# Performance work log

Hardware: AMD Instinct MI355X
Metric: run time of the kernel (lower is better)

Reference implementation:

```python
import jax, jax.numpy as jnp
import numpy as np

PATCH = 14
DIM = 512
LEVELS = 6
ITERS = LEVELS * 2  # default iters
TOKEN_ATTEND_SELF_VALUE = -0.0005


def setup_inputs() -> dict:
    key = jax.random.key(0)
    ks = jax.random.split(key, 9)
    b = 8
    # weights scaled down (~1/sqrt(dim)) so 12 iterations stay finite in fp32
    s = 0.02
    return {
        "img": jax.random.normal(ks[0], (b, 3, 224, 224), jnp.float32),
        "W_patch": jax.random.normal(ks[1], (PATCH * PATCH * 3, DIM), jnp.float32) * s,
        "b_patch": jax.random.normal(ks[2], (DIM,), jnp.float32) * s,
        "pos_emb": jax.random.normal(ks[3], (256, DIM), jnp.float32) * s,
        "init_levels": jax.random.normal(ks[4], (LEVELS, DIM), jnp.float32),
        "bu_in": jax.random.normal(ks[5], (LEVELS - 1, DIM, 4 * DIM), jnp.float32) * s,
        "bu_out": jax.random.normal(ks[6], (LEVELS - 1, 4 * DIM, DIM), jnp.float32) * s,
        "td_in": jax.random.normal(ks[7], (LEVELS - 1, DIM, 4 * DIM), jnp.float32) * s,
        "td_out": jax.random.normal(ks[8], (LEVELS - 1, 4 * DIM, DIM), jnp.float32) * s,
    }


def _grouped_ff(x, w_in, w_out):
    # x: [b, n, groups, d]; per-group two-layer FF with exact GELU
    h = jnp.einsum('bnld,lde->bnle', x, w_in)
    h = jax.nn.gelu(h, approximate=False)
    return jnp.einsum('bnld,lde->bnle', h, w_out)


def _consensus(levels):
    # levels: [b, n, l, d]; attend_self=False, no local radius
    n, d = levels.shape[1], levels.shape[-1]
    norm = jnp.maximum(jnp.linalg.norm(levels, axis=-1, keepdims=True), 1e-12)
    k = levels / norm
    sim = jnp.einsum('bild,bjld->blij', levels, k) * (d ** -0.5)
    eye = jnp.eye(n, dtype=bool)[None, None]
    sim = jnp.where(eye, jnp.asarray(TOKEN_ATTEND_SELF_VALUE, sim.dtype), sim)
    attn = jax.nn.softmax(sim, axis=-1)
    return jnp.einsum('blij,bjld->bild', attn, levels)


def reference(img, W_patch, b_patch, pos_emb, init_levels, bu_in, bu_out, td_in, td_out):
    b, c, H, W = img.shape
    p = PATCH
    h, w = H // p, W // p
    # 'b c (h p1) (w p2) -> b (h w) (p1 p2 c)'
    x = img.reshape(b, c, h, p, w, p).transpose(0, 2, 4, 3, 5, 1).reshape(b, h * w, p * p * c)
    tokens = x @ W_patch + b_patch  # [b, n, d]
    n = tokens.shape[1]
    pos = pos_emb[:n][None, :, None, :]       # [1, n, 1, d]
    bottom = tokens[:, :, None, :]            # [b, n, 1, d]
    levels = jnp.broadcast_to(init_levels[None, None], (b, n, LEVELS, DIM))

    for _ in range(ITERS):
        lwi = jnp.concatenate([bottom, levels], axis=2)            # [b, n, L+1, d]
        bu = _grouped_ff(lwi[:, :, 1:-1], bu_in, bu_out)           # [b, n, L-1, d]
        td = _grouped_ff(lwi[:, :, 2:] + pos, td_in, td_out)       # [b, n, L-1, d]
        bu = jnp.concatenate([bottom, bu], axis=2)                 # [b, n, L, d]
        td = jnp.pad(td, ((0, 0), (0, 0), (0, 1), (0, 0)))         # [b, n, L, d]
        cons = _consensus(levels)
        levels = (levels + bu + td + cons) * 0.25
    return levels
```

## Files before the change

### kernel.cpp

```cpp
#include <hip/hip_runtime.h>
#include <hip/hip_bf16.h>
#include <math.h>

#define B_   8
#define N_   256
#define L_   6
#define D_   512
#define NT_  2048
#define HID_ 2048

typedef __attribute__((ext_vector_type(4))) float f32x4;
typedef __attribute__((ext_vector_type(8))) short bf16x8;

struct bf16x4s { __hip_bfloat16 x, y, z, w; };

__device__ __forceinline__ bf16x4s to_bf4(float a, float b, float c, float d) {
    bf16x4s r;
    r.x = __float2bfloat16(a); r.y = __float2bfloat16(b);
    r.z = __float2bfloat16(c); r.w = __float2bfloat16(d);
    return r;
}

__device__ __forceinline__ float bf_to_f(unsigned short u) {
    union { unsigned int i; float f; } c;
    c.i = ((unsigned int)u) << 16;
    return c.f;
}

__device__ __forceinline__ void gload16(const void* g, void* l) {
    __builtin_amdgcn_global_load_lds(
        (const __attribute__((address_space(1))) int*)g,
        (__attribute__((address_space(3))) int*)l, 16, 0, 0);
}

__device__ __forceinline__ float gelu_exact(float v) {
    return 0.5f * v * (1.0f + erff(v * 0.70710678118654752f));
}

template<int BM, int BN, int WM, int WN, typename CT, bool GELU>
__global__ __launch_bounds__(512, 4) void gemm_ff(
    const __hip_bfloat16* __restrict__ A1, int lda1, long az1,
    const __hip_bfloat16* __restrict__ A2, int lda2, long az2, int zsplit,
    const __hip_bfloat16* __restrict__ B, int ldb, long bz,
    CT* __restrict__ C, int ldc, long cz, int K)
{
    constexpr int WVM = BM / WM, WVN = BN / WN;
    constexpr int MR = WVM / 16, NR = WVN / 16;
    constexpr int ALOADS = (BM * 64) / (512 * 8);
    constexpr int BLOADS = (BN * 64) / (512 * 8);
    constexpr int LOADS  = ALOADS + BLOADS;

    __shared__ short As[2][BM * 64];
    __shared__ short Bs[2][BN * 64];

    const int tid = threadIdx.x;
    const int wv = tid >> 6, lane = tid & 63;
    const int wr = wv / WN, wc = wv % WN;

    const int gx = gridDim.x, gy = gridDim.y;
    const int nwg = gx * gy * gridDim.z;
    int lid = (blockIdx.z * gy + blockIdx.y) * gx + blockIdx.x;
    lid = (lid & 7) * (nwg >> 3) + (lid >> 3);
    const int bx = lid % gx, by = (lid / gx) % gy, bzz = lid / (gx * gy);

    const __hip_bfloat16* A;
    int lda;
    if (bzz < zsplit) { A = A1 + (long)bzz * az1;            lda = lda1; }
    else              { A = A2 + (long)(bzz - zsplit) * az2; lda = lda2; }
    B += (long)bzz * bz;  C += (long)bzz * cz;
    const int m0 = by * BM, n0 = bx * BN;

    f32x4 acc[MR][NR] = {};

    const int srow_a = tid >> 3, sslot = tid & 7;

#define STAGE(BUF, K0)                                                        \
    {                                                                         \
        _Pragma("unroll")                                                     \
        for (int i = 0; i < ALOADS; ++i) {                                    \
            const int row = srow_a + i * 64;                                  \
            const int gs  = sslot ^ (row & 7);                                \
            gload16(A + (long)(m0 + row) * lda + (K0) + gs * 8,               \
                    &As[BUF][(wv * 64 + i * 512) * 8]);                       \
        }                                                                     \
        _Pragma("unroll")                                                     \
        for (int i = 0; i < BLOADS; ++i) {                                    \
            const int row = srow_a + i * 64;                                  \
            const int gs  = sslot ^ (row & 7);                                \
            gload16(B + (long)(n0 + row) * ldb + (K0) + gs * 8,               \
                    &Bs[BUF][(wv * 64 + i * 512) * 8]);                       \
        }                                                                     \
    }

    const int fr = lane & 15, k4 = lane >> 4;
    const int nt = K / 64;
    int cur = 0;

    STAGE(0, 0);

    for (int t = 0; t < nt; ++t) {
        if (t + 1 < nt) {
            STAGE(cur ^ 1, (t + 1) * 64);
            asm volatile("s_waitcnt vmcnt(%0)\n\ts_barrier"
                         :: "n"(LOADS) : "memory");
        } else {
            asm volatile("s_waitcnt vmcnt(0)\n\ts_barrier" ::: "memory");
        }

#pragma unroll
        for (int ks = 0; ks < 2; ++ks) {
            bf16x8 af[MR], bf[NR];
#pragma unroll
            for (int i = 0; i < MR; ++i) {
                const int r = wr * WVM + i * 16 + fr;
                af[i] = *(const bf16x8*)&As[cur][r * 64 + ((ks * 4 + k4) ^ (r & 7)) * 8];
            }
#pragma unroll
            for (int j = 0; j < NR; ++j) {
                const int r = wc * WVN + j * 16 + fr;
                bf[j] = *(const bf16x8*)&Bs[cur][r * 64 + ((ks * 4 + k4) ^ (r & 7)) * 8];
            }
            __builtin_amdgcn_s_setprio(1);
#pragma unroll
            for (int i = 0; i < MR; ++i)
#pragma unroll
                for (int j = 0; j < NR; ++j)
                    acc[i][j] = __builtin_amdgcn_mfma_f32_16x16x32_bf16(
                        af[i], bf[j], acc[i][j], 0, 0, 0);
            __builtin_amdgcn_s_setprio(0);
        }
        asm volatile("s_waitcnt lgkmcnt(0)\n\ts_barrier" ::: "memory");
        cur ^= 1;
    }
#undef STAGE

    const int cr4 = (lane >> 4) * 4, cc = lane & 15;
#pragma unroll
    for (int i = 0; i < MR; ++i)
#pragma unroll
        for (int j = 0; j < NR; ++j) {
            const int col = n0 + wc * WVN + j * 16 + cc;
#pragma unroll
            for (int r = 0; r < 4; ++r) {
                const int row = m0 + wr * WVM + i * 16 + cr4 + r;
                float v = acc[i][j][r];
                if (GELU) v = gelu_exact(v);
                CT* p = &C[(long)row * ldc + col];
                if constexpr (sizeof(CT) == 2) *p = __float2bfloat16(v);
                else *p = (CT)v;
            }
        }
}

__global__ __launch_bounds__(256) void simsm_kernel(
    const __hip_bfloat16* __restrict__ lev_bf, const float* __restrict__ invn,
    __hip_bfloat16* __restrict__ attn)
{
    __shared__ short As[64 * 32];
    __shared__ short Bs[256 * 32];
    __shared__ float redm[64][4];
    __shared__ float reds[64][4];

    const int tid = threadIdx.x;
    const int wv = tid >> 6, lane = tid & 63;
    const int z = blockIdx.y;
    const int b = z / 6, l = z - 6 * b;
    const __hip_bfloat16* base = lev_bf + (long)b * (N_ * L_ * D_) + (long)l * D_;
    const int m0 = blockIdx.x * 64;

    const int srow = tid >> 2, sslot = tid & 3;

    f32x4 acc[4][4] = {};
    const int fr = lane & 15, ksub = lane >> 4;

    for (int k0 = 0; k0 < 512; k0 += 32) {
        __syncthreads();
        {
            const int gs = sslot ^ ((srow >> 1) & 3);
            gload16(base + (long)(m0 + srow) * (L_ * D_) + k0 + gs * 8,
                    As + wv * 512);
        }
#pragma unroll
        for (int i = 0; i < 4; ++i) {
            const int row = srow + i * 64;
            const int gs  = sslot ^ ((row >> 1) & 3);
            gload16(base + (long)row * (L_ * D_) + k0 + gs * 8,
                    Bs + i * 2048 + wv * 512);
        }
        __syncthreads();

        bf16x8 af[4], bfr[4];
#pragma unroll
        for (int i = 0; i < 4; ++i) {
            const int ra = i * 16 + fr;
            af[i] = *(const bf16x8*)(As + ra * 32 + (ksub ^ ((ra >> 1) & 3)) * 8);
            const int rb = wv * 64 + i * 16 + fr;
            bfr[i] = *(const bf16x8*)(Bs + rb * 32 + (ksub ^ ((rb >> 1) & 3)) * 8);
        }
#pragma unroll
        for (int i = 0; i < 4; ++i)
#pragma unroll
            for (int j = 0; j < 4; ++j)
                acc[i][j] = __builtin_amdgcn_mfma_f32_16x16x32_bf16(
                    af[i], bfr[j], acc[i][j], 0, 0, 0);
    }

    const int cr4 = (lane >> 4) * 4, cc = lane & 15;
    const float sc = 0.044194173824159216f;

    float iv[4];
#pragma unroll
    for (int j = 0; j < 4; ++j)
        iv[j] = invn[((long)b * N_ + wv * 64 + j * 16 + cc) * L_ + l] * sc;
#pragma unroll
    for (int i = 0; i < 4; ++i)
#pragma unroll
        for (int j = 0; j < 4; ++j) {
            const int jg = wv * 64 + j * 16 + cc;
#pragma unroll
            for (int r = 0; r < 4; ++r) {
                const int ig = m0 + i * 16 + cr4 + r;
                float v = acc[i][j][r] * iv[j];
                if (ig == jg) v = -0.0005f;
                acc[i][j][r] = v;
            }
        }

    __syncthreads();

#pragma unroll
    for (int i = 0; i < 4; ++i)
#pragma unroll
        for (int r = 0; r < 4; ++r) {
            float m = fmaxf(fmaxf(acc[i][0][r], acc[i][1][r]),
                            fmaxf(acc[i][2][r], acc[i][3][r]));
#pragma unroll
            for (int o = 1; o < 16; o <<= 1) m = fmaxf(m, __shfl_xor(m, o));
            if (cc == 0) redm[i * 16 + cr4 + r][wv] = m;
        }
    __syncthreads();

#pragma unroll
    for (int i = 0; i < 4; ++i)
#pragma unroll
        for (int r = 0; r < 4; ++r) {
            const int rl = i * 16 + cr4 + r;
            const float m = fmaxf(fmaxf(redm[rl][0], redm[rl][1]),
                                  fmaxf(redm[rl][2], redm[rl][3]));
            float s = 0.f;
#pragma unroll
            for (int j = 0; j < 4; ++j) {
                const float e = expf(acc[i][j][r] - m);
                acc[i][j][r] = e;
                s += e;
            }
#pragma unroll
            for (int o = 1; o < 16; o <<= 1) s += __shfl_xor(s, o);
            if (cc == 0) reds[rl][wv] = s;
        }
    __syncthreads();

#pragma unroll
    for (int i = 0; i < 4; ++i)
#pragma unroll
        for (int r = 0; r < 4; ++r) {
            const int rl = i * 16 + cr4 + r;
            const float inv = 1.0f / (reds[rl][0] + reds[rl][1] +
                                      reds[rl][2] + reds[rl][3]);
            const long rowoff = ((long)z * N_ + m0 + rl) * N_;
#pragma unroll
            for (int j = 0; j < 4; ++j)
                attn[rowoff + wv * 64 + j * 16 + cc] =
                    __float2bfloat16(acc[i][j][r] * inv);
        }
}

__device__ __forceinline__ void mfma_kloop(
    const __hip_bfloat16* __restrict__ A, int lda,
    const __hip_bfloat16* __restrict__ B, int ldb,
    int m0, int n0, int K, short* As, short* Bs,
    f32x4 acc[4][4], int wave, int lane)
{
    const int srow_in = lane >> 2;
    const int sslot   = lane & 3;
    const int wm = (wave >> 1) * 64, wn = (wave & 1) * 64;

    for (int k0 = 0; k0 < K; k0 += 32) {
        __syncthreads();
#pragma unroll
        for (int c = 0; c < 2; ++c) {
            const int rbase = c * 64 + wave * 16;
            const int row   = rbase + srow_in;
            const int gk    = sslot ^ ((row >> 1) & 3);
            gload16(A + (long)(m0 + row) * lda + k0 + gk * 8, As + rbase * 32);
            gload16(B + (long)(n0 + row) * ldb + k0 + gk * 8, Bs + rbase * 32);
        }
        __syncthreads();

        const int fr = lane & 15, ksub = lane >> 4;
        bf16x8 af[4], bfr[4];
#pragma unroll
        for (int i = 0; i < 4; ++i) {
            const int ra = wm + i * 16 + fr;
            af[i]  = *(const bf16x8*)(As + ra * 32 + (ksub ^ ((ra >> 1) & 3)) * 8);
            const int rb = wn + i * 16 + fr;
            bfr[i] = *(const bf16x8*)(Bs + rb * 32 + (ksub ^ ((rb >> 1) & 3)) * 8);
        }
#pragma unroll
        for (int i = 0; i < 4; ++i)
#pragma unroll
            for (int j = 0; j < 4; ++j)
                acc[i][j] = __builtin_amdgcn_mfma_f32_16x16x32_bf16(
                    af[i], bfr[j], acc[i][j], 0, 0, 0);
    }
}

template<typename CT, bool GELU>
__global__ __launch_bounds__(256) void gemm_mfma(
    const __hip_bfloat16* __restrict__ A, int lda, long az,
    const __hip_bfloat16* __restrict__ B, int ldb, long bz,
    CT* __restrict__ C, int ldc, long cz, int K,
    const float* __restrict__ bias)
{
    __shared__ short As[128 * 32];
    __shared__ short Bs[128 * 32];
    const int tid = threadIdx.x;
    const int wave = tid >> 6, lane = tid & 63;
    const int z = blockIdx.z;
    A += (long)z * az;  B += (long)z * bz;  C += (long)z * cz;
    const int m0 = blockIdx.y * 128, n0 = blockIdx.x * 128;
    const int wm = (wave >> 1) * 64, wn = (wave & 1) * 64;

    f32x4 acc[4][4] = {};
    mfma_kloop(A, lda, B, ldb, m0, n0, K, As, Bs, acc, wave, lane);

    const int cr = lane >> 4, cc = lane & 15;
#pragma unroll
    for (int j = 0; j < 4; ++j) {
        const int col = n0 + wn + j * 16 + cc;
        const float bv = bias ? bias[col] : 0.f;
#pragma unroll
        for (int i = 0; i < 4; ++i)
#pragma unroll
            for (int r = 0; r < 4; ++r) {
                const int row = m0 + wm + i * 16 + cr * 4 + r;
                float v = acc[i][j][r] + bv;
                if (GELU) v = gelu_exact(v);
                CT* p = &C[(long)row * ldc + col];
                if constexpr (sizeof(CT) == 2) *p = __float2bfloat16(v);
                else *p = (CT)v;
            }
    }
}

__global__ __launch_bounds__(256) void cons_mfma(
    const __hip_bfloat16* __restrict__ attn, const __hip_bfloat16* __restrict__ levT,
    __hip_bfloat16* __restrict__ cons)
{
    __shared__ short As[128 * 32];
    __shared__ short Bs[128 * 32];
    const int tid = threadIdx.x;
    const int wave = tid >> 6, lane = tid & 63;
    const int z = blockIdx.z;
    const int b = z / 6, l = z - 6 * b;
    const __hip_bfloat16* A = attn + (long)z * N_ * N_;
    const __hip_bfloat16* B = levT + (long)z * D_ * N_;
    __hip_bfloat16* C = cons + (long)b * (N_ * L_ * D_) + (long)l * D_;
    const int m0 = blockIdx.y * 128, n0 = blockIdx.x * 128;
    const int wm = (wave >> 1) * 64, wn = (wave & 1) * 64;

    f32x4 acc[4][4] = {};
    mfma_kloop(A, N_, B, N_, m0, n0, N_, As, Bs, acc, wave, lane);

    const int cr = lane >> 4, cc = lane & 15;
#pragma unroll
    for (int j = 0; j < 4; ++j) {
        const int col = n0 + wn + j * 16 + cc;
#pragma unroll
        for (int i = 0; i < 4; ++i)
#pragma unroll
            for (int r = 0; r < 4; ++r) {
                const int row = m0 + wm + i * 16 + cr * 4 + r;
                C[(long)row * (L_ * D_) + col] = __float2bfloat16(acc[i][j][r]);
            }
    }
}

__global__ __launch_bounds__(256) void transpose_to_bf16(
    const float* __restrict__ src, __hip_bfloat16* __restrict__ dst,
    int R, int Cc)
{
    __shared__ float t[32][33];
    const int zz = blockIdx.z;
    src += (long)zz * R * Cc;  dst += (long)zz * R * Cc;
    const int tx = threadIdx.x & 31, ty = threadIdx.x >> 5;
    const int c0 = blockIdx.x * 32, r0 = blockIdx.y * 32;
#pragma unroll
    for (int i = 0; i < 4; ++i)
        t[ty + i * 8][tx] = src[(long)(r0 + ty + i * 8) * Cc + c0 + tx];
    __syncthreads();
#pragma unroll
    for (int i = 0; i < 4; ++i)
        dst[(long)(c0 + ty + i * 8) * R + r0 + tx] = __float2bfloat16(t[tx][ty + i * 8]);
}

__global__ __launch_bounds__(256) void levT_kernel(
    const float* __restrict__ levels, __hip_bfloat16* __restrict__ levT)
{
    __shared__ float t[32][33];
    const int z = blockIdx.z;
    const int b = z / 6, l = z - 6 * b;
    const float* base = levels + (long)b * (N_ * L_ * D_) + (long)l * D_;
    const int tx = threadIdx.x & 31, ty = threadIdx.x >> 5;
    const int d0 = blockIdx.x * 32, j0 = blockIdx.y * 32;
#pragma unroll
    for (int i = 0; i < 4; ++i)
        t[ty + i * 8][tx] = base[(long)(j0 + ty + i * 8) * (L_ * D_) + d0 + tx];
    __syncthreads();
#pragma unroll
    for (int i = 0; i < 4; ++i)
        levT[(long)z * D_ * N_ + (long)(d0 + ty + i * 8) * N_ + j0 + tx] =
            __float2bfloat16(t[tx][ty + i * 8]);
}

__global__ __launch_bounds__(256) void invnorm_kernel(
    const float* __restrict__ levels, float* __restrict__ invn)
{
    const int wid = blockIdx.x * 4 + (threadIdx.x >> 6);
    const int lane = threadIdx.x & 63;
    const float* row = levels + (long)wid * 512;
    float s = 0.f;
#pragma unroll
    for (int k = lane * 4; k < 512; k += 256) {
        const float4 v = *(const float4*)&row[k];
        s += v.x * v.x + v.y * v.y + v.z * v.z + v.w * v.w;
    }
#pragma unroll
    for (int o = 1; o < 64; o <<= 1) s += __shfl_xor(s, o);
    if (lane == 0) invn[wid] = 1.0f / fmaxf(sqrtf(s), 1e-12f);
}

__global__ __launch_bounds__(256) void patchify_kernel(
    const float* __restrict__ img, __hip_bfloat16* __restrict__ Xp)
{
    const int t = blockIdx.x;
    const int b = t >> 8, n = t & 255;
    const int hh = n >> 4, ww = n & 15;
    for (int k = threadIdx.x; k < 608; k += 256) {
        float v = 0.f;
        if (k < 588) {
            const int c = k % 3;
            const int pj = (k / 3) % 14;
            const int pi = k / 42;
            v = img[(((long)b * 3 + c) * 224 + (hh * 14 + pi)) * 224 + (ww * 14 + pj)];
        }
        Xp[(long)t * 608 + k] = __float2bfloat16(v);
    }
}

__global__ __launch_bounds__(256) void wpT_kernel(
    const float* __restrict__ Wp, __hip_bfloat16* __restrict__ WpT)
{
    __shared__ float t[32][33];
    const int k0 = blockIdx.x * 32, d0 = blockIdx.y * 32;
    const int tx = threadIdx.x & 31, ty = threadIdx.x >> 5;
#pragma unroll
    for (int i = 0; i < 4; ++i) {
        const int k = k0 + ty + i * 8;
        t[ty + i * 8][tx] = (k < 588) ? Wp[(long)k * 512 + d0 + tx] : 0.f;
    }
    __syncthreads();
#pragma unroll
    for (int i = 0; i < 4; ++i)
        WpT[(long)(d0 + ty + i * 8) * 608 + k0 + tx] = __float2bfloat16(t[tx][ty + i * 8]);
}

__global__ __launch_bounds__(256) void init_levels_kernel(
    float* __restrict__ levels, const float* __restrict__ initlv)
{
    const long f = (long)blockIdx.x * 256 + threadIdx.x;
    const int d4 = f & 127;
    const int l = (int)((f >> 7) % 6);
    *(float4*)&levels[f * 4] = *(const float4*)&initlv[(long)l * 512 + d4 * 4];
}

__global__ __launch_bounds__(256) void lev_lp_init(
    const float* __restrict__ levels, const float* __restrict__ pos,
    __hip_bfloat16* __restrict__ lev_bf, __hip_bfloat16* __restrict__ lp_bf)
{
    const long f = (long)blockIdx.x * 256 + threadIdx.x;
    const int d4 = f & 127;
    const long tl = f >> 7;
    const int l = (int)(tl % 6);
    const long t = tl / 6;
    const float4 v = *(const float4*)&levels[f * 4];
    *(bf16x4s*)&lev_bf[f * 4] = to_bf4(v.x, v.y, v.z, v.w);
    if (l >= 1) {
        const float4 p = *(const float4*)&pos[(long)(t & 255) * 512 + d4 * 4];
        *(bf16x4s*)&lp_bf[((t * 5 + l - 1) * 512) + d4 * 4] =
            to_bf4(v.x + p.x, v.y + p.y, v.z + p.z, v.w + p.w);
    }
}

__global__ __launch_bounds__(256) void update_kernel(
    float* __restrict__ levels, const float* __restrict__ tokens,
    const __hip_bfloat16* __restrict__ acc_bu, const __hip_bfloat16* __restrict__ acc_td,
    const __hip_bfloat16* __restrict__ cons, const float* __restrict__ pos,
    __hip_bfloat16* __restrict__ lev_bf, __hip_bfloat16* __restrict__ lp_bf,
    float* __restrict__ invn)
{
    const int wid = blockIdx.x * 4 + (threadIdx.x >> 6);
    const int lane = threadIdx.x & 63;
    const int l = wid % 6;
    const long t = wid / 6;
    const long rowoff = (long)wid * 512;

    float ss = 0.f;
#pragma unroll
    for (int half = 0; half < 2; ++half) {
        const int k = lane * 4 + half * 256;
        const long off = rowoff + k;
        float4 lev = *(const float4*)&levels[off];
        const ushort4 cu = *(const ushort4*)&cons[off];
        float4 ac;
        if (l == 0) {
            ac = *(const float4*)&tokens[t * 512 + k];
        } else {
            const ushort4 bu = *(const ushort4*)&acc_bu[((long)(l - 1) * NT_ + t) * 512 + k];
            ac = make_float4(bf_to_f(bu.x), bf_to_f(bu.y), bf_to_f(bu.z), bf_to_f(bu.w));
        }
        if (l < 5) {
            const ushort4 td = *(const ushort4*)&acc_td[((long)l * NT_ + t) * 512 + k];
            ac.x += bf_to_f(td.x); ac.y += bf_to_f(td.y);
            ac.z += bf_to_f(td.z); ac.w += bf_to_f(td.w);
        }
        lev.x = (lev.x + ac.x + bf_to_f(cu.x)) * 0.25f;
        lev.y = (lev.y + ac.y + bf_to_f(cu.y)) * 0.25f;
        lev.z = (lev.z + ac.z + bf_to_f(cu.z)) * 0.25f;
        lev.w = (lev.w + ac.w + bf_to_f(cu.w)) * 0.25f;
        *(float4*)&levels[off] = lev;
        *(bf16x4s*)&lev_bf[off] = to_bf4(lev.x, lev.y, lev.z, lev.w);
        if (l >= 1) {
            const float4 p = *(const float4*)&pos[(long)(t & 255) * 512 + k];
            *(bf16x4s*)&lp_bf[((t * 5 + l - 1) * 512) + k] =
                to_bf4(lev.x + p.x, lev.y + p.y, lev.z + p.z, lev.w + p.w);
        }
        ss += lev.x * lev.x + lev.y * lev.y + lev.z * lev.z + lev.w * lev.w;
    }
#pragma unroll
    for (int o = 1; o < 64; o <<= 1) ss += __shfl_xor(ss, o);
    if (lane == 0) invn[wid] = 1.0f / fmaxf(sqrtf(ss), 1e-12f);
}

extern "C" void kernel_launch(void* const* d_in, const int* in_sizes, int n_in,
                              void* d_out, int out_size, void* d_ws, size_t ws_size,
                              hipStream_t stream)
{
    const float* img    = (const float*)d_in[0];
    const float* Wp     = (const float*)d_in[1];
    const float* bp     = (const float*)d_in[2];
    const float* pos    = (const float*)d_in[3];
    const float* initlv = (const float*)d_in[4];
    const float* bu_in  = (const float*)d_in[5];
    const float* bu_out = (const float*)d_in[6];
    const float* td_in  = (const float*)d_in[7];
    const float* td_out = (const float*)d_in[8];

    float* levels = (float*)d_out;
    float* ws = (float*)d_ws;
    float* tokens  = ws;
    __hip_bfloat16* acc_bu = (__hip_bfloat16*)(tokens + 1048576);
    __hip_bfloat16* acc_td = acc_bu + 5242880;
    __hip_bfloat16* h = acc_td + 5242880;
    float* invn    = (float*)(h + 41943040);
    __hip_bfloat16* lev_bf   = (__hip_bfloat16*)(invn + 12288);
    __hip_bfloat16* lp_bf    = lev_bf + 6291456;
    __hip_bfloat16* wtin_all = lp_bf + 5242880;
    __hip_bfloat16* wtout_all= wtin_all + 10485760;

    __hip_bfloat16* cons_bf = h;
    __hip_bfloat16* levT_bf = lev_bf;
    __hip_bfloat16* attn_bf = lp_bf;
    __hip_bfloat16* Xp  = acc_bu;
    __hip_bfloat16* WpT = Xp + 1245184;

    init_levels_kernel<<<6144, 256, 0, stream>>>(levels, initlv);
    lev_lp_init<<<6144, 256, 0, stream>>>(levels, pos, lev_bf, lp_bf);
    invnorm_kernel<<<3072, 256, 0, stream>>>(levels, invn);
    patchify_kernel<<<NT_, 256, 0, stream>>>(img, Xp);
    wpT_kernel<<<dim3(19, 16), 256, 0, stream>>>(Wp, WpT);
    gemm_mfma<float, false><<<dim3(4, 16, 1), 256, 0, stream>>>(
        Xp, 608, 0, WpT, 608, 0, tokens, 512, 0, 608, bp);
    transpose_to_bf16<<<dim3(64, 16, 5), 256, 0, stream>>>(bu_in,  wtin_all, 512, 2048);
    transpose_to_bf16<<<dim3(64, 16, 5), 256, 0, stream>>>(td_in,  wtin_all + 5242880, 512, 2048);
    transpose_to_bf16<<<dim3(16, 64, 5), 256, 0, stream>>>(bu_out, wtout_all, 2048, 512);
    transpose_to_bf16<<<dim3(16, 64, 5), 256, 0, stream>>>(td_out, wtout_all + 5242880, 2048, 512);

    for (int it = 0; it < 12; ++it) {
        gemm_ff<128, 128, 2, 4, __hip_bfloat16, true>
            <<<dim3(16, 16, 10), 512, 0, stream>>>(
            lev_bf, L_ * D_, 512,
            lp_bf, 5 * D_, 512, 5,
            wtin_all, D_, (long)HID_ * D_,
            h, HID_, (long)NT_ * HID_, D_);
        gemm_ff<128, 128, 2, 4, __hip_bfloat16, false>
            <<<dim3(4, 16, 10), 512, 0, stream>>>(
            h, HID_, (long)NT_ * HID_,
            h, HID_, (long)NT_ * HID_, 10,
            wtout_all, HID_, (long)D_ * HID_,
            acc_bu, D_, (long)NT_ * D_, HID_);

        simsm_kernel<<<dim3(4, 48), 256, 0, stream>>>(lev_bf, invn, attn_bf);
        levT_kernel<<<dim3(16, 8, 48), 256, 0, stream>>>(levels, levT_bf);
        cons_mfma<<<dim3(4, 2, 48), 256, 0, stream>>>(attn_bf, levT_bf, cons_bf);
        update_kernel<<<3072, 256, 0, stream>>>(levels, tokens, acc_bu, acc_td,
                                                cons_bf, pos, lev_bf, lp_bf, invn);
    }
}
```

Baseline: 2.324 ms.

## Add 256x256-tile 8-wave GEMM with quadrant ping-pong for FF input layer

Adds a new grouped GEMM kernel that computes 256x256 output tiles per workgroup as four 128x128 quadrants, double-buffering LDS halves and interleaving async global-to-LDS loads between MFMA phases, with XCD-aware block remapping and priority bumps around MFMA bursts. The first FF GEMM (input projection with GELU) switches to it, using an 8x8x10 grid. The larger tile raises operand reuse per LDS byte and is meant to reduce global traffic and barrier overhead. In exchange it uses much more LDS and many registers (launch bounds of 2 per CU), there are only 640 workgroups, and the fine-grained vmcnt/barrier scheduling is fragile.

```diff
diff --git a/kernel.cpp b/kernel.cpp
--- a/kernel.cpp
+++ b/kernel.cpp
@@ -35,6 +35,148 @@
 
 __device__ __forceinline__ float gelu_exact(float v) {
     return 0.5f * v * (1.0f + erff(v * 0.70710678118654752f));
+}
+
+template<typename CT, bool GELU>
+__global__ __launch_bounds__(512, 2) void gemm_ff8(
+    const __hip_bfloat16* __restrict__ A1p, int lda1, long az1,
+    const __hip_bfloat16* __restrict__ A2p, int lda2, long az2, int zsplit,
+    const __hip_bfloat16* __restrict__ B, int ldb, long bz,
+    CT* __restrict__ C, int ldc, long cz, int K)
+{
+    __shared__ short SA[2][2][128 * 64];
+    __shared__ short SB[2][2][128 * 64];
+
+    const int tid = threadIdx.x;
+    const int wv = tid >> 6, lane = tid & 63;
+    const int wr = wv >> 2, wc = wv & 3;
+
+    const int gx = gridDim.x, gy = gridDim.y;
+    const int nwg = gx * gy * gridDim.z;
+    int lid = (blockIdx.z * gy + blockIdx.y) * gx + blockIdx.x;
+    lid = (lid & 7) * (nwg >> 3) + (lid >> 3);
+    const int bx = lid % gx, by = (lid / gx) % gy, bzz = lid / (gx * gy);
+
+    const __hip_bfloat16* A;
+    int lda;
+    if (bzz < zsplit) { A = A1p + (long)bzz * az1;            lda = lda1; }
+    else              { A = A2p + (long)(bzz - zsplit) * az2; lda = lda2; }
+    B += (long)bzz * bz;  C += (long)bzz * cz;
+    const int m0 = by * 256, n0 = bx * 256;
+
+    const int srow = tid >> 3, sslot = tid & 7;
+    const int fr = lane & 15, k4 = lane >> 4;
+
+    f32x4 acc[2][2][4][2] = {};
+    bf16x8 af[4][2];
+    bf16x8 bf[2][2][2];
+
+#define STAGE_HALF(S, P, LD, BR, BUF, HF, K0)                                 \
+    {                                                                         \
+        _Pragma("unroll")                                                     \
+        for (int i_ = 0; i_ < 2; ++i_) {                                      \
+            const int r_ = srow + i_ * 64;                                    \
+            const int gs_ = sslot ^ (r_ & 7);                                 \
+            gload16(P + (long)((BR) + r_) * (LD) + (K0) + gs_ * 8,            \
+                    &S[BUF][HF][(i_ * 64 + wv * 8) * 64]);                    \
+        }                                                                     \
+    }
+
+#define READ_A(QM, BUF)                                                       \
+    {                                                                         \
+        _Pragma("unroll")                                                     \
+        for (int i_ = 0; i_ < 4; ++i_) {                                      \
+            const int r_ = wr * 64 + i_ * 16 + fr;                            \
+            af[i_][0] = *(const bf16x8*)&SA[BUF][QM][r_ * 64 + ((k4)     ^ (r_ & 7)) * 8]; \
+            af[i_][1] = *(const bf16x8*)&SA[BUF][QM][r_ * 64 + ((4 + k4) ^ (r_ & 7)) * 8]; \
+        }                                                                     \
+    }
+
+#define READ_B(QN, BUF)                                                       \
+    {                                                                         \
+        _Pragma("unroll")                                                     \
+        for (int j_ = 0; j_ < 2; ++j_) {                                      \
+            const int r_ = wc * 32 + j_ * 16 + fr;                            \
+            bf[QN][j_][0] = *(const bf16x8*)&SB[BUF][QN][r_ * 64 + ((k4)     ^ (r_ & 7)) * 8]; \
+            bf[QN][j_][1] = *(const bf16x8*)&SB[BUF][QN][r_ * 64 + ((4 + k4) ^ (r_ & 7)) * 8]; \
+        }                                                                     \
+    }
+
+#define MFMA_PHASE(QM, QN)                                                    \
+    __builtin_amdgcn_s_barrier();                                             \
+    asm volatile("s_waitcnt lgkmcnt(0)" ::: "memory");                        \
+    __builtin_amdgcn_sched_barrier(0);                                        \
+    __builtin_amdgcn_s_setprio(1);                                            \
+    {                                                                         \
+        _Pragma("unroll")                                                     \
+        for (int i_ = 0; i_ < 4; ++i_)                                        \
+            _Pragma("unroll")                                                 \
+            for (int j_ = 0; j_ < 2; ++j_) {                                  \
+                acc[QM][QN][i_][j_] = __builtin_amdgcn_mfma_f32_16x16x32_bf16(\
+                    af[i_][0], bf[QN][j_][0], acc[QM][QN][i_][j_], 0, 0, 0);  \
+                acc[QM][QN][i_][j_] = __builtin_amdgcn_mfma_f32_16x16x32_bf16(\
+                    af[i_][1], bf[QN][j_][1], acc[QM][QN][i_][j_], 0, 0, 0);  \
+            }                                                                 \
+    }                                                                         \
+    __builtin_amdgcn_s_setprio(0);
+
+    STAGE_HALF(SA, A, lda, m0 + 0,   0, 0, 0);
+    STAGE_HALF(SB, B, ldb, n0 + 0,   0, 0, 0);
+    STAGE_HALF(SA, A, lda, m0 + 128, 0, 1, 0);
+    STAGE_HALF(SB, B, ldb, n0 + 128, 0, 1, 0);
+    STAGE_HALF(SA, A, lda, m0 + 0,   1, 0, 64);
+    STAGE_HALF(SB, B, ldb, n0 + 0,   1, 0, 64);
+    STAGE_HALF(SB, B, ldb, n0 + 128, 1, 1, 64);
+    asm volatile("s_waitcnt vmcnt(6)" ::: "memory");
+    __builtin_amdgcn_s_barrier();
+
+    const int nt = K / 64;
+    for (int t = 0; t < nt; ++t) {
+        const int buf = t & 1, nbuf = buf ^ 1;
+        const int k2 = (t + 2) * 64;
+        READ_A(0, buf);
+        READ_B(0, buf);
+        if (t + 1 < nt) STAGE_HALF(SA, A, lda, m0 + 128, nbuf, 1, (t + 1) * 64);
+        MFMA_PHASE(0, 0);
+        __builtin_amdgcn_s_barrier();
+        READ_B(1, buf);
+        if (t + 2 < nt) STAGE_HALF(SA, A, lda, m0 + 0, buf, 0, k2);
+        MFMA_PHASE(0, 1);
+        __builtin_amdgcn_s_barrier();
+        READ_A(1, buf);
+        if (t + 2 < nt) STAGE_HALF(SB, B, ldb, n0 + 0, buf, 0, k2);
+        MFMA_PHASE(1, 0);
+        __builtin_amdgcn_s_barrier();
+        if (t + 2 < nt) STAGE_HALF(SB, B, ldb, n0 + 128, buf, 1, k2);
+        MFMA_PHASE(1, 1);
+        asm volatile("s_waitcnt vmcnt(6)" ::: "memory");
+        __builtin_amdgcn_s_barrier();
+    }
+#undef STAGE_HALF
+#undef READ_A
+#undef READ_B
+#undef MFMA_PHASE
+
+    const int cr4 = (lane >> 4) * 4, cc = lane & 15;
+#pragma unroll
+    for (int qm = 0; qm < 2; ++qm)
+#pragma unroll
+        for (int qn = 0; qn < 2; ++qn)
+#pragma unroll
+            for (int i = 0; i < 4; ++i)
+#pragma unroll
+                for (int j = 0; j < 2; ++j) {
+                    const int col = n0 + qn * 128 + wc * 32 + j * 16 + cc;
+#pragma unroll
+                    for (int r = 0; r < 4; ++r) {
+                        const int row = m0 + qm * 128 + wr * 64 + i * 16 + cr4 + r;
+                        float v = acc[qm][qn][i][j][r];
+                        if (GELU) v = gelu_exact(v);
+                        CT* p = &C[(long)row * ldc + col];
+                        if constexpr (sizeof(CT) == 2) *p = __float2bfloat16(v);
+                        else *p = (CT)v;
+                    }
+                }
 }
 
 template<int BM, int BN, int WM, int WN, typename CT, bool GELU>
@@ -597,8 +739,8 @@
     transpose_to_bf16<<<dim3(16, 64, 5), 256, 0, stream>>>(td_out, wtout_all + 5242880, 2048, 512);
 
     for (int it = 0; it < 12; ++it) {
-        gemm_ff<128, 128, 2, 4, __hip_bfloat16, true>
-            <<<dim3(16, 16, 10), 512, 0, stream>>>(
+        gemm_ff8<__hip_bfloat16, true>
+            <<<dim3(8, 8, 10), 512, 0, stream>>>(
             lev_bf, L_ * D_, 512,
             lp_bf, 5 * D_, 512, 5,
             wtin_all, D_, (long)HID_ * D_,
```

Measured after the change: 2.480 ms. +6.7%, slower.
